# Kernel optimization log

Hardware: AMD Instinct MI355X
Metric: run time of the kernel (lower is better)

## Reference

```python
import jax, jax.numpy as jnp
import numpy as np

D_MODEL = 1024
N_HEADS = 16
D_K = D_MODEL // N_HEADS


def setup_inputs() -> dict:
    key = jax.random.key(0)
    ks = jax.random.split(key, 7)
    B, S = 2, 2048
    q = jax.random.normal(ks[0], (B, S, D_MODEL), dtype=jnp.float32)
    k = jax.random.normal(ks[1], (B, S, D_MODEL), dtype=jnp.float32)
    v = jax.random.normal(ks[2], (B, S, D_MODEL), dtype=jnp.float32)
    mask = jnp.ones((B, 1, S, S), dtype=bool)
    scale = 1.0 / np.sqrt(D_MODEL)
    w_q = jax.random.normal(ks[3], (D_MODEL, D_MODEL), dtype=jnp.float32) * scale
    w_k = jax.random.normal(ks[4], (D_MODEL, D_MODEL), dtype=jnp.float32) * scale
    w_v = jax.random.normal(ks[5], (D_MODEL, D_MODEL), dtype=jnp.float32) * scale
    w_o = jax.random.normal(ks[6], (D_MODEL, D_MODEL), dtype=jnp.float32) * scale
    return {"q": q, "k": k, "v": v, "mask": mask,
            "w_q": w_q, "w_k": w_k, "w_v": w_v, "w_o": w_o}


def reference(q, k, v, mask, w_q, w_k, w_v, w_o):
    B, S, _ = q.shape
    # projections (nn.Linear: x @ W^T, no bias)
    def split_heads(x):  # [B,S,D] -> [B,H,S,d_k]
        return x.reshape(B, -1, N_HEADS, D_K).transpose(0, 2, 1, 3)
    query = split_heads(q @ w_q.T)
    key_h = split_heads(k @ w_k.T)
    value = split_heads(v @ w_v.T)
    # naive scaled dot-product attention: full [B,H,S,S] scores materialized
    scores = jnp.einsum('bhqd,bhkd->bhqk', query, key_h) / jnp.sqrt(
        jnp.asarray(D_K, query.dtype))
    scores = jnp.where(mask, scores, jnp.asarray(-1e9, scores.dtype))
    attn = jax.nn.softmax(scores, axis=-1)  # dropout p=0.0 -> identity
    x = jnp.einsum('bhqk,bhkd->bhqd', attn, value)
    x = x.transpose(0, 2, 1, 3).reshape(B, S, N_HEADS * D_K)
    return x @ w_o.T
```

## Files before the change

kernel.cpp:

```cpp
#include <hip/hip_runtime.h>
#include <hip/hip_bf16.h>
#include <math.h>

typedef __bf16 bf16;
typedef __bf16 bf16x8 __attribute__((ext_vector_type(8)));
typedef float f32x4 __attribute__((ext_vector_type(4)));
typedef float f32x16 __attribute__((ext_vector_type(16)));
typedef unsigned u32x4 __attribute__((ext_vector_type(4)));

#define MFMA16(a, b, c) __builtin_amdgcn_mfma_f32_16x16x32_bf16((a), (b), (c), 0, 0, 0)
#define MFMA32(a, b, c) __builtin_amdgcn_mfma_f32_32x32x16_bf16((a), (b), (c), 0, 0, 0)

__device__ __forceinline__ void gl_lds16(const void* g, void* l) {
    __builtin_amdgcn_global_load_lds(
        (__attribute__((address_space(1))) void*)(g),
        (__attribute__((address_space(3))) void*)(l),
        16, 0, 0);
}

__device__ __forceinline__ unsigned cvt_pk_bf16(float lo, float hi) {
    unsigned r;
    asm("v_cvt_pk_bf16_f32 %0, %1, %2" : "=v"(r) : "v"(lo), "v"(hi));
    return r;
}

__global__ __launch_bounds__(256) void cvt7(
    const float* __restrict__ w0, const float* __restrict__ w1,
    const float* __restrict__ w2, const float* __restrict__ w3,
    const float* __restrict__ x0, const float* __restrict__ x1,
    const float* __restrict__ x2, bf16* __restrict__ dst) {
    const int z = blockIdx.y;
    const float* src;
    bf16* out;
    if (z < 4) {
        if (blockIdx.x >= 512) return;
        src = (z == 0) ? w0 : (z == 1) ? w1 : (z == 2) ? w2 : w3;
        out = dst + (size_t)z * 1048576;
    } else {
        src = (z == 4) ? x0 : (z == 5) ? x1 : x2;
        out = dst + 4 * 1048576 + (size_t)(z - 4) * 4194304;
    }
    const int i = (blockIdx.x * 256 + threadIdx.x) * 8;
    float4 a = ((const float4*)(src + i))[0];
    float4 b = ((const float4*)(src + i))[1];
    bf16x8 o;
    o[0] = (bf16)a.x; o[1] = (bf16)a.y; o[2] = (bf16)a.z; o[3] = (bf16)a.w;
    o[4] = (bf16)b.x; o[5] = (bf16)b.y; o[6] = (bf16)b.z; o[7] = (bf16)b.w;
    *(bf16x8*)(out + i) = o;
}

template <int EP>
__device__ __forceinline__ void gemm_bf(const bf16* __restrict__ A,
                                        const bf16* __restrict__ B,
                                        void* __restrict__ Cv,
                                        const int m0, const int n0) {
    constexpr int K = 1024;
    __shared__ __align__(16) bf16 As[128 * 32];
    __shared__ __align__(16) bf16 Bs[128 * 32];

    const int t = threadIdx.x;
    const int lane = t & 63;
    const int w = t >> 6;
    const int wm = (w & 1) * 64;
    const int wn = (w >> 1) * 64;
    const int lr = lane & 15;
    const int lq8 = (lane >> 4) * 8;
    const int rq = (lane >> 4) * 4;

    f32x4 acc[4][4] = {};

    const int srow = t >> 2;
    const int sch = (t & 3) * 8;
    char* lA = (char*)As;
    char* lB = (char*)Bs;

    for (int k0 = 0; k0 < K; k0 += 32) {
        gl_lds16(A + (size_t)(m0 + srow) * K + k0 + sch,      lA + t * 16);
        gl_lds16(A + (size_t)(m0 + 64 + srow) * K + k0 + sch, lA + 4096 + t * 16);
        gl_lds16(B + (size_t)(n0 + srow) * K + k0 + sch,      lB + t * 16);
        gl_lds16(B + (size_t)(n0 + 64 + srow) * K + k0 + sch, lB + 4096 + t * 16);
        __syncthreads();

        bf16x8 af[4], bfr[4];
#pragma unroll
        for (int i = 0; i < 4; ++i) {
            af[i]  = *(const bf16x8*)&As[(wm + i * 16 + lr) * 32 + lq8];
            bfr[i] = *(const bf16x8*)&Bs[(wn + i * 16 + lr) * 32 + lq8];
        }
#pragma unroll
        for (int mi = 0; mi < 4; ++mi)
#pragma unroll
            for (int ni = 0; ni < 4; ++ni)
                acc[mi][ni] = MFMA16(af[mi], bfr[ni], acc[mi][ni]);
        __syncthreads();
    }

#pragma unroll
    for (int mi = 0; mi < 4; ++mi) {
#pragma unroll
        for (int ni = 0; ni < 4; ++ni) {
#pragma unroll
            for (int r = 0; r < 4; ++r) {
                const int m = m0 + wm + mi * 16 + rq + r;
                const int n = n0 + wn + ni * 16 + lr;
                const float vv = acc[mi][ni][r];
                if constexpr (EP == 0) {
                    bf16* C = (bf16*)Cv;
                    const int b = m >> 11, s = m & 2047;
                    const int h = n >> 6,  d = n & 63;
                    C[(((size_t)(b * 16 + h)) * 2048 + s) * 64 + d] = (bf16)vv;
                } else if constexpr (EP == 1) {
                    float* C = (float*)Cv;
                    C[(size_t)m * 1024 + n] = vv;
                } else {
                    bf16* C = (bf16*)Cv;
                    C[((size_t)(n >> 11) * 1024 + m) * 2048 + (n & 2047)] = (bf16)vv;
                }
            }
        }
    }
}

__global__ __launch_bounds__(256, 3) void qkv_bf(
    const bf16* __restrict__ Xq, const bf16* __restrict__ Xk,
    const bf16* __restrict__ Xv, const bf16* __restrict__ Wc,
    bf16* __restrict__ Qb, bf16* __restrict__ Kb, bf16* __restrict__ Vb) {
    const int z = blockIdx.z;
    if (z == 0)
        gemm_bf<0>(Xq, Wc, Qb, blockIdx.x * 128, blockIdx.y * 128);
    else if (z == 1)
        gemm_bf<0>(Xk, Wc + 1048576, Kb, blockIdx.x * 128, blockIdx.y * 128);
    else
        gemm_bf<2>(Wc + 2 * 1048576, Xv, Vb, blockIdx.y * 128, blockIdx.x * 128);
}

__global__ __launch_bounds__(256, 2) void out_gemm(
    const bf16* __restrict__ X, const bf16* __restrict__ W, float* __restrict__ C) {
    gemm_bf<1>(X, W, C, blockIdx.x * 128, blockIdx.y * 128);
}

template <int MODE>
__device__ __forceinline__ void gemm_f32tok(const void* __restrict__ Av,
                                            const void* __restrict__ Bv,
                                            bf16* __restrict__ C,
                                            const int m0, const int n0) {
    constexpr int K = 1024;
    __shared__ __align__(16) bf16 As[128 * 32];
    __shared__ __align__(16) bf16 Bs[128 * 32];

    const int t = threadIdx.x;
    const int lane = t & 63;
    const int w = t >> 6;
    const int wm = (w & 1) * 64;
    const int wn = (w >> 1) * 64;
    const int lr = lane & 15;
    const int lq8 = (lane >> 4) * 8;
    const int rq = (lane >> 4) * 4;

    f32x4 acc[4][4] = {};
    const int srow = t >> 2;
    const int sch = (t & 3) * 8;
    const int ar = t >> 1;
    const int ac = (t & 1) * 16;
    char* lA = (char*)As;
    char* lB = (char*)Bs;

    for (int k0 = 0; k0 < K; k0 += 32) {
        if constexpr (MODE == 0) {
            const float* X = (const float*)Av;
            const float* p = X + (size_t)(m0 + ar) * K + k0 + ac;
            float4 f0 = ((const float4*)p)[0], f1 = ((const float4*)p)[1];
            float4 f2 = ((const float4*)p)[2], f3 = ((const float4*)p)[3];
            bf16x8 o0, o1;
            o0[0]=(bf16)f0.x; o0[1]=(bf16)f0.y; o0[2]=(bf16)f0.z; o0[3]=(bf16)f0.w;
            o0[4]=(bf16)f1.x; o0[5]=(bf16)f1.y; o0[6]=(bf16)f1.z; o0[7]=(bf16)f1.w;
            o1[0]=(bf16)f2.x; o1[1]=(bf16)f2.y; o1[2]=(bf16)f2.z; o1[3]=(bf16)f2.w;
            o1[4]=(bf16)f3.x; o1[5]=(bf16)f3.y; o1[6]=(bf16)f3.z; o1[7]=(bf16)f3.w;
            *(bf16x8*)&As[ar * 32 + ac]     = o0;
            *(bf16x8*)&As[ar * 32 + ac + 8] = o1;
        } else {
            const bf16* X = (const bf16*)Av;
            gl_lds16(X + (size_t)(m0 + srow) * K + k0 + sch,      lA + t * 16);
            gl_lds16(X + (size_t)(m0 + 64 + srow) * K + k0 + sch, lA + 4096 + t * 16);
        }
        if constexpr (MODE == 2) {
            const float* X = (const float*)Bv;
            const float* p = X + (size_t)(n0 + ar) * K + k0 + ac;
            float4 f0 = ((const float4*)p)[0], f1 = ((const float4*)p)[1];
            float4 f2 = ((const float4*)p)[2], f3 = ((const float4*)p)[3];
            bf16x8 o0, o1;
            o0[0]=(bf16)f0.x; o0[1]=(bf16)f0.y; o0[2]=(bf16)f0.z; o0[3]=(bf16)f0.w;
            o0[4]=(bf16)f1.x; o0[5]=(bf16)f1.y; o0[6]=(bf16)f1.z; o0[7]=(bf16)f1.w;
            o1[0]=(bf16)f2.x; o1[1]=(bf16)f2.y; o1[2]=(bf16)f2.z; o1[3]=(bf16)f2.w;
            o1[4]=(bf16)f3.x; o1[5]=(bf16)f3.y; o1[6]=(bf16)f3.z; o1[7]=(bf16)f3.w;
            *(bf16x8*)&Bs[ar * 32 + ac]     = o0;
            *(bf16x8*)&Bs[ar * 32 + ac + 8] = o1;
        } else {
            const bf16* W = (const bf16*)Bv;
            gl_lds16(W + (size_t)(n0 + srow) * K + k0 + sch,      lB + t * 16);
            gl_lds16(W + (size_t)(n0 + 64 + srow) * K + k0 + sch, lB + 4096 + t * 16);
        }
        __syncthreads();

        bf16x8 af[4], bfr[4];
#pragma unroll
        for (int i = 0; i < 4; ++i) {
            af[i]  = *(const bf16x8*)&As[(wm + i * 16 + lr) * 32 + lq8];
            bfr[i] = *(const bf16x8*)&Bs[(wn + i * 16 + lr) * 32 + lq8];
        }
#pragma unroll
        for (int mi = 0; mi < 4; ++mi)
#pragma unroll
            for (int ni = 0; ni < 4; ++ni)
                acc[mi][ni] = MFMA16(af[mi], bfr[ni], acc[mi][ni]);
        __syncthreads();
    }

#pragma unroll
    for (int mi = 0; mi < 4; ++mi) {
#pragma unroll
        for (int ni = 0; ni < 4; ++ni) {
#pragma unroll
            for (int r = 0; r < 4; ++r) {
                const int m = m0 + wm + mi * 16 + rq + r;
                const int n = n0 + wn + ni * 16 + lr;
                const float vv = acc[mi][ni][r];
                if constexpr (MODE == 0) {
                    const int b = m >> 11, s = m & 2047;
                    const int h = n >> 6,  d = n & 63;
                    C[(((size_t)(b * 16 + h)) * 2048 + s) * 64 + d] = (bf16)vv;
                } else {
                    C[((size_t)(n >> 11) * 1024 + m) * 2048 + (n & 2047)] = (bf16)vv;
                }
            }
        }
    }
}

__global__ __launch_bounds__(256, 2) void qkv_f32(
    const float* __restrict__ q, const float* __restrict__ k, const float* __restrict__ v,
    const bf16* __restrict__ Wc, bf16* __restrict__ Qb, bf16* __restrict__ Kb,
    bf16* __restrict__ Vb) {
    const int z = blockIdx.z;
    if (z == 0)
        gemm_f32tok<0>(q, Wc, Qb, blockIdx.x * 128, blockIdx.y * 128);
    else if (z == 1)
        gemm_f32tok<0>(k, Wc + 1048576, Kb, blockIdx.x * 128, blockIdx.y * 128);
    else
        gemm_f32tok<2>(Wc + 2 * 1048576, v, Vb, blockIdx.y * 128, blockIdx.x * 128);
}

__global__ __launch_bounds__(512, 2) void attn_kernel(
    const bf16* __restrict__ Qb, const bf16* __restrict__ Kb,
    const bf16* __restrict__ Vb, bf16* __restrict__ Xb) {
    constexpr int S = 2048;

    __shared__ __align__(16) bf16 Ks[32 * 128];
    __shared__ __align__(16) bf16 Vs[32 * 128];

    const int t = threadIdx.x;
    const int lane = t & 63;
    const int w = t >> 6;
    const int l31 = lane & 31;
    const int half = lane >> 5;
    const int bh = blockIdx.y;
    const int q0 = blockIdx.x * 256 + w * 32;
    const bf16* Q  = Qb + (size_t)bh * S * 64;
    const bf16* Kh = Kb + (size_t)bh * S * 64;
    const bf16* Vh = Vb + (size_t)bh * 64 * S;

    const float qscale = 0.125f * 1.4426950408889634f;
    bf16x8 qf[4];
#pragma unroll
    for (int c = 0; c < 4; ++c) {
        bf16x8 v0 = *(const bf16x8*)(Q + (size_t)(q0 + l31) * 64 + c * 16 + half * 8);
#pragma unroll
        for (int e = 0; e < 8; ++e) v0[e] = (bf16)((float)v0[e] * qscale);
        qf[c] = v0;
    }

    f32x16 od[2] = {};
    float ls0 = 0.f, ls1 = 0.f, ls2 = 0.f, ls3 = 0.f;

    const int sr = t >> 3;
    const int cg = t & 7;
    const bf16* pKg = Kh + (size_t)sr * 64 + cg * 8;
    const bf16* pVg = Vh + (size_t)sr * S + cg * 8;
    const int wK = (sr >> 1) * 128 + ((((sr & 1) << 3) + cg) ^ ((sr >> 1) & 15)) * 8;

    bf16x8 pk, pv;
    pk = *(const bf16x8*)pKg;
    pv = *(const bf16x8*)pVg;

    const int fbase = (l31 >> 1) * 128;
    const int fb8 = (l31 & 1) << 3;
    const int fsw = l31 >> 1;

    for (int j = 0; j < S / 64; ++j) {
        __syncthreads();
        *(bf16x8*)&Ks[wK] = pk;
        *(bf16x8*)&Vs[wK] = pv;
        __syncthreads();

        f32x16 sacc[2] = {};
#pragma unroll
        for (int kt = 0; kt < 2; ++kt) {
#pragma unroll
            for (int c = 0; c < 4; ++c) {
                bf16x8 kf = *(const bf16x8*)
                    &Ks[kt * 2048 + fbase + ((fb8 + c * 2 + half) ^ fsw) * 8];
                sacc[kt] = MFMA32(kf, qf[c], sacc[kt]);
            }
        }

        if (j + 1 < S / 64) {
            pKg += 4096;
            pVg += 64;
            pk = *(const bf16x8*)pKg;
            pv = *(const bf16x8*)pVg;
        }

#pragma unroll
        for (int kt = 0; kt < 2; ++kt) {
            float ex[16];
#pragma unroll
            for (int r = 0; r < 16; ++r)
                ex[r] = exp2f(sacc[kt][r]);
            ls0 += ex[0] + ex[4] + ex[8]  + ex[12];
            ls1 += ex[1] + ex[5] + ex[9]  + ex[13];
            ls2 += ex[2] + ex[6] + ex[10] + ex[14];
            ls3 += ex[3] + ex[7] + ex[11] + ex[15];

            unsigned pa[8];
#pragma unroll
            for (int c2 = 0; c2 < 2; ++c2) {
#pragma unroll
                for (int wd = 0; wd < 2; ++wd) {
                    unsigned x = cvt_pk_bf16(ex[c2 * 8 + wd * 2 + 0], ex[c2 * 8 + wd * 2 + 1]);
                    unsigned y = cvt_pk_bf16(ex[c2 * 8 + wd * 2 + 4], ex[c2 * 8 + wd * 2 + 5]);
                    asm("v_permlane32_swap_b32 %0, %1" : "+v"(x), "+v"(y));
                    pa[c2 * 4 + wd]     = x;
                    pa[c2 * 4 + wd + 2] = y;
                }
            }

#pragma unroll
            for (int c2 = 0; c2 < 2; ++c2) {
                u32x4 aw;
                aw[0] = pa[c2 * 4 + 0]; aw[1] = pa[c2 * 4 + 1];
                aw[2] = pa[c2 * 4 + 2]; aw[3] = pa[c2 * 4 + 3];
                bf16x8 ap = __builtin_bit_cast(bf16x8, aw);
#pragma unroll
                for (int dt = 0; dt < 2; ++dt) {
                    const int cgv = kt * 4 + c2 * 2 + half;
                    bf16x8 vf = *(const bf16x8*)
                        &Vs[dt * 2048 + fbase + ((fb8 + cgv) ^ fsw) * 8];
                    od[dt] = MFMA32(ap, vf, od[dt]);
                }
            }
        }
    }

    float lsum = ls0 + ls1 + ls2 + ls3;
    const float ltot = lsum + __shfl_xor(lsum, 32);
    const float inv = 1.f / fmaxf(ltot, 1e-30f);
    const int b = bh >> 4, hh = bh & 15;
#pragma unroll
    for (int r = 0; r < 16; ++r) {
        const int qrow = (r & 3) + 8 * (r >> 2) + 4 * half;
        const float invr = __shfl(inv, qrow);
        const size_t base = ((size_t)(b * 2048 + q0 + qrow)) * 1024 + hh * 64;
        Xb[base + l31]      = (bf16)(od[0][r] * invr);
        Xb[base + 32 + l31] = (bf16)(od[1][r] * invr);
    }
}

extern "C" void kernel_launch(void* const* d_in, const int* in_sizes, int n_in,
                              void* d_out, int out_size, void* d_ws, size_t ws_size,
                              hipStream_t stream) {
    const float* q  = (const float*)d_in[0];
    const float* k  = (const float*)d_in[1];
    const float* v  = (const float*)d_in[2];
    const float* wq = (const float*)d_in[4];
    const float* wk = (const float*)d_in[5];
    const float* wv = (const float*)d_in[6];
    const float* wo = (const float*)d_in[7];
    float* out = (float*)d_out;

    const bool big = ws_size >= (size_t)64 * 1024 * 1024;
    bf16* Wc = (bf16*)d_ws;
    const dim3 blk(256);

    if (big) {
        bf16* Xq = Wc + 4 * 1048576;
        bf16* Xk = Xq + 4194304;
        bf16* Xv = Xk + 4194304;
        bf16* Qb = Xv + 4194304;
        bf16* Kb = Qb + 4194304;
        bf16* Vb = Kb + 4194304;
        bf16* Xb = Vb + 4194304;
        cvt7<<<dim3(2048, 7), blk, 0, stream>>>(wq, wk, wv, wo, q, k, v, Wc);
        qkv_bf<<<dim3(32, 8, 3), blk, 0, stream>>>(Xq, Xk, Xv, Wc, Qb, Kb, Vb);
        attn_kernel<<<dim3(8, 32), dim3(512), 0, stream>>>(Qb, Kb, Vb, Xb);
        out_gemm<<<dim3(32, 8), blk, 0, stream>>>(Xb, Wc + 3 * 1048576, out);
    } else {
        bf16* Qb = Wc + 4 * 1048576;
        bf16* Kb = Qb + 4194304;
        bf16* Vb = Kb + 4194304;
        bf16* Xb = Vb + 4194304;
        cvt7<<<dim3(512, 4), blk, 0, stream>>>(wq, wk, wv, wo, q, k, v, Wc);
        qkv_f32<<<dim3(32, 8, 3), blk, 0, stream>>>(q, k, v, Wc, Qb, Kb, Vb);
        attn_kernel<<<dim3(8, 32), dim3(512), 0, stream>>>(Qb, Kb, Vb, Xb);
        out_gemm<<<dim3(32, 8), blk, 0, stream>>>(Xb, Wc + 3 * 1048576, out);
    }
}
```

Baseline: 234.8 us.

## Split attention keys across two wave groups and merge partial outputs in LDS

The attention kernel now gives each block 128 queries, with two groups of four waves each covering half of the key sequence (1024 keys). Partial output accumulators and row sums from the second group are combined through shared memory before the normalized write. The launch grows from 256 to 512 blocks and a linearized block index groups heads for cache locality. The aim is more parallelism and better CU fill with the 256-CU device. The cost is an extra LDS reduction step and per-thread loads that are twice as wide, which add register pressure.

Result: no change. 237.9 us (+1.3%).

```diff
diff --git a/kernel.cpp b/kernel.cpp
--- a/kernel.cpp
+++ b/kernel.cpp
@@ -250,21 +250,26 @@
         gemm_f32tok<2>(Wc + 2 * 1048576, v, Vb, blockIdx.y * 128, blockIdx.x * 128);
 }
 
-__global__ __launch_bounds__(512, 2) void attn_kernel(
+__global__ __launch_bounds__(512, 4) void attn_kernel(
     const bf16* __restrict__ Qb, const bf16* __restrict__ Kb,
     const bf16* __restrict__ Vb, bf16* __restrict__ Xb) {
     constexpr int S = 2048;
 
-    __shared__ __align__(16) bf16 Ks[32 * 128];
-    __shared__ __align__(16) bf16 Vs[32 * 128];
+    __shared__ __align__(16) bf16 smem[17408];
 
     const int t = threadIdx.x;
     const int lane = t & 63;
     const int w = t >> 6;
+    const int wg = w & 3;
+    const int kh = w >> 2;
     const int l31 = lane & 31;
     const int half = lane >> 5;
-    const int bh = blockIdx.y;
-    const int q0 = blockIdx.x * 256 + w * 32;
+
+    const int lin = blockIdx.x;
+    const int g = lin >> 3;
+    const int bh = (lin & 7) + 8 * (g & 3);
+    const int q0 = (g >> 2) * 128 + wg * 32;
+
     const bf16* Q  = Qb + (size_t)bh * S * 64;
     const bf16* Kh = Kb + (size_t)bh * S * 64;
     const bf16* Vh = Vb + (size_t)bh * 64 * S;
@@ -282,24 +287,36 @@
     f32x16 od[2] = {};
     float ls0 = 0.f, ls1 = 0.f, ls2 = 0.f, ls3 = 0.f;
 
-    const int sr = t >> 3;
-    const int cg = t & 7;
-    const bf16* pKg = Kh + (size_t)sr * 64 + cg * 8;
-    const bf16* pVg = Vh + (size_t)sr * S + cg * 8;
-    const int wK = (sr >> 1) * 128 + ((((sr & 1) << 3) + cg) ^ ((sr >> 1) & 15)) * 8;
-
-    bf16x8 pk, pv;
-    pk = *(const bf16x8*)pKg;
-    pv = *(const bf16x8*)pVg;
+    const int tt = t & 255;
+    const int sr = tt >> 2;
+    const int sc = (tt & 3) * 2;
+    const bf16* pKg = Kh + ((size_t)kh * 1024 + sr) * 64 + sc * 8;
+    const bf16* pVg = Vh + (size_t)sr * S + kh * 1024 + sc * 8;
+    bf16* KsH = smem + kh * 4096;
+    bf16* VsH = smem + 8192 + kh * 4096;
+    int wKo[2];
+#pragma unroll
+    for (int c = 0; c < 2; ++c)
+        wKo[c] = (sr >> 1) * 128 + ((((sr & 1) << 3) + sc + c) ^ ((sr >> 1) & 15)) * 8;
+
+    bf16x8 pk[2], pv[2];
+#pragma unroll
+    for (int c = 0; c < 2; ++c) {
+        pk[c] = *(const bf16x8*)(pKg + c * 8);
+        pv[c] = *(const bf16x8*)(pVg + c * 8);
+    }
 
     const int fbase = (l31 >> 1) * 128;
     const int fb8 = (l31 & 1) << 3;
     const int fsw = l31 >> 1;
 
-    for (int j = 0; j < S / 64; ++j) {
-        __syncthreads();
-        *(bf16x8*)&Ks[wK] = pk;
-        *(bf16x8*)&Vs[wK] = pv;
+    for (int j = 0; j < 16; ++j) {
+        __syncthreads();
+#pragma unroll
+        for (int c = 0; c < 2; ++c) {
+            *(bf16x8*)&KsH[wKo[c]] = pk[c];
+            *(bf16x8*)&VsH[wKo[c]] = pv[c];
+        }
         __syncthreads();
 
         f32x16 sacc[2] = {};
@@ -308,16 +325,19 @@
 #pragma unroll
             for (int c = 0; c < 4; ++c) {
                 bf16x8 kf = *(const bf16x8*)
-                    &Ks[kt * 2048 + fbase + ((fb8 + c * 2 + half) ^ fsw) * 8];
+                    &KsH[kt * 2048 + fbase + ((fb8 + c * 2 + half) ^ fsw) * 8];
                 sacc[kt] = MFMA32(kf, qf[c], sacc[kt]);
             }
         }
 
-        if (j + 1 < S / 64) {
+        if (j + 1 < 16) {
             pKg += 4096;
             pVg += 64;
-            pk = *(const bf16x8*)pKg;
-            pv = *(const bf16x8*)pVg;
+#pragma unroll
+            for (int c = 0; c < 2; ++c) {
+                pk[c] = *(const bf16x8*)(pKg + c * 8);
+                pv[c] = *(const bf16x8*)(pVg + c * 8);
+            }
         }
 
 #pragma unroll
@@ -354,7 +374,7 @@
                 for (int dt = 0; dt < 2; ++dt) {
                     const int cgv = kt * 4 + c2 * 2 + half;
                     bf16x8 vf = *(const bf16x8*)
-                        &Vs[dt * 2048 + fbase + ((fb8 + cgv) ^ fsw) * 8];
+                        &VsH[dt * 2048 + fbase + ((fb8 + cgv) ^ fsw) * 8];
                     od[dt] = MFMA32(ap, vf, od[dt]);
                 }
             }
@@ -362,16 +382,32 @@
     }
 
     float lsum = ls0 + ls1 + ls2 + ls3;
-    const float ltot = lsum + __shfl_xor(lsum, 32);
-    const float inv = 1.f / fmaxf(ltot, 1e-30f);
-    const int b = bh >> 4, hh = bh & 15;
-#pragma unroll
-    for (int r = 0; r < 16; ++r) {
-        const int qrow = (r & 3) + 8 * (r >> 2) + 4 * half;
-        const float invr = __shfl(inv, qrow);
-        const size_t base = ((size_t)(b * 2048 + q0 + qrow)) * 1024 + hh * 64;
-        Xb[base + l31]      = (bf16)(od[0][r] * invr);
-        Xb[base + 32 + l31] = (bf16)(od[1][r] * invr);
+    float ltot = lsum + __shfl_xor(lsum, 32);
+
+    __syncthreads();
+    float* fsm = (float*)smem;
+    const int so = (wg * 64 + lane) * 34;
+    if (kh == 1) {
+        fsm[so + 32] = ltot;
+#pragma unroll
+        for (int r = 0; r < 16; ++r) {
+            fsm[so + r]      = od[0][r];
+            fsm[so + 16 + r] = od[1][r];
+        }
+    }
+    __syncthreads();
+    if (kh == 0) {
+        ltot += fsm[so + 32];
+        const float inv = 1.f / fmaxf(ltot, 1e-30f);
+        const int b = bh >> 4, hh = bh & 15;
+#pragma unroll
+        for (int r = 0; r < 16; ++r) {
+            const int qrow = (r & 3) + 8 * (r >> 2) + 4 * half;
+            const float invr = __shfl(inv, qrow);
+            const size_t base = ((size_t)(b * 2048 + q0 + qrow)) * 1024 + hh * 64;
+            Xb[base + l31]      = (bf16)((od[0][r] + fsm[so + r]) * invr);
+            Xb[base + 32 + l31] = (bf16)((od[1][r] + fsm[so + 16 + r]) * invr);
+        }
     }
 }
 
@@ -401,7 +437,7 @@
         bf16* Xb = Vb + 4194304;
         cvt7<<<dim3(2048, 7), blk, 0, stream>>>(wq, wk, wv, wo, q, k, v, Wc);
         qkv_bf<<<dim3(32, 8, 3), blk, 0, stream>>>(Xq, Xk, Xv, Wc, Qb, Kb, Vb);
-        attn_kernel<<<dim3(8, 32), dim3(512), 0, stream>>>(Qb, Kb, Vb, Xb);
+        attn_kernel<<<dim3(512), dim3(512), 0, stream>>>(Qb, Kb, Vb, Xb);
         out_gemm<<<dim3(32, 8), blk, 0, stream>>>(Xb, Wc + 3 * 1048576, out);
     } else {
         bf16* Qb = Wc + 4 * 1048576;
@@ -410,7 +446,7 @@
         bf16* Xb = Vb + 4194304;
         cvt7<<<dim3(512, 4), blk, 0, stream>>>(wq, wk, wv, wo, q, k, v, Wc);
         qkv_f32<<<dim3(32, 8, 3), blk, 0, stream>>>(q, k, v, Wc, Qb, Kb, Vb);
-        attn_kernel<<<dim3(8, 32), dim3(512), 0, stream>>>(Qb, Kb, Vb, Xb);
+        attn_kernel<<<dim3(512), dim3(512), 0, stream>>>(Qb, Kb, Vb, Xb);
         out_gemm<<<dim3(32, 8), blk, 0, stream>>>(Xb, Wc + 3 * 1048576, out);
     }
 }
```
